# Optimization experiments

Measured on AMD Instinct MI355X. Metric: run time of the kernel, lower is better.

The kernel has to match this reference:

```python
import jax, jax.numpy as jnp
import numpy as np

N, K, D = 65536, 1024, 256
COMMIT = 0.25
EPS = 1e-12


def setup_inputs() -> dict:
    key = jax.random.key(0)
    kx, kw = jax.random.split(key)
    x = jax.random.normal(kx, (N, D), dtype=jnp.float32)
    # nn.Embedding weight init: uniform(-1/vector_num, 1/vector_num)
    weight = jax.random.uniform(kw, (K, D), dtype=jnp.float32,
                                minval=-1.0 / K, maxval=1.0 / K)
    return {"x": x, "weight": weight}


def reference(x, weight):
    distances = (jnp.sum(x * x, axis=1, keepdims=True)
                 + jnp.sum(weight * weight, axis=1)
                 - 2.0 * (x @ weight.T))
    vector_indices = jnp.argmin(distances, axis=1)              # [N]
    quantized = weight[vector_indices]                          # gather == one-hot @ weight

    e_latent_loss = jnp.mean((jax.lax.stop_gradient(quantized) - x) ** 2)
    q_latent_loss = jnp.mean((quantized - jax.lax.stop_gradient(x)) ** 2)
    quant_loss = q_latent_loss + COMMIT * e_latent_loss

    # straight-through estimator
    quantized_out = x + jax.lax.stop_gradient(quantized - x)

    # utilization: counts of each code (== column sums of one-hot encodings)
    counts = jnp.zeros((K,), x.dtype).at[vector_indices].add(1.0)
    util_loss = jnp.mean(jnp.abs(counts - x.shape[0] / K))

    # compactness: 2 * mean of pairwise euclidean distances among codebook rows
    sq = jnp.sum(weight * weight, axis=1)
    pd2 = sq[:, None] + sq[None, :] - 2.0 * (weight @ weight.T)  # [K, K]
    iu = jnp.triu(jnp.ones((K, K), bool), 1)
    pd = jnp.sqrt(jnp.maximum(jnp.where(iu, pd2, 1.0), EPS))
    n_pairs = K * (K - 1) // 2
    compact_loss = 2.0 * jnp.sum(jnp.where(iu, pd, 0.0)) / n_pairs

    return quantized_out, quant_loss, util_loss, compact_loss, vector_indices
```

## Files before the change

kernel.cpp:

```cpp
#include <hip/hip_runtime.h>
#include <math.h>

#define NROWS 65536
#define KCODES 1024
#define DDIM 256
#define ND_TOT (NROWS * DDIM)

#define WS_IDX      0
#define WS_COUNTS   262144
#define WS_SW       266240
#define WS_PARTQ    532480
#define WS_PARTP    536576
#define WS_FLAGCNT  540672
#define WS_FLAGLIST 540928
#define WS_WH       803072
#define WS_WL       1327360

typedef float f32x4 __attribute__((ext_vector_type(4)));
typedef short bf16x8 __attribute__((ext_vector_type(8)));

__device__ inline unsigned short f2bf(float f) {
  unsigned u = __float_as_uint(f);
  u += 0x7FFFu + ((u >> 16) & 1u);
  return (unsigned short)(u >> 16);
}
__device__ inline float bf2f(unsigned short h) {
  return __uint_as_float(((unsigned)h) << 16);
}

__device__ inline void gload16(const void* g, void* l) {
  __builtin_amdgcn_global_load_lds((const __attribute__((address_space(1))) void*)g,
                                   (__attribute__((address_space(3))) void*)l, 16, 0, 0);
}

__global__ __launch_bounds__(256) void vq_prep(const float* __restrict__ x,
                                               const float* __restrict__ w,
                                               unsigned short* __restrict__ xh,
                                               unsigned short* __restrict__ xl,
                                               float* __restrict__ sw,
                                               unsigned short* __restrict__ wh,
                                               unsigned short* __restrict__ wl,
                                               int* __restrict__ counts,
                                               int* __restrict__ flagCnt) {
#pragma clang fp contract(off)
  const int b = blockIdx.x;
  const int t = threadIdx.x;
  if (b >= 2048) {
    const int lane = t & 63, wv = t >> 6;
    const int row = (b - 2048) * 4 + wv;
    const float* src = w + (size_t)row * DDIM;
    float4 v4 = *(const float4*)&src[lane * 4];
    float fv[4] = {v4.x, v4.y, v4.z, v4.w};
    union { unsigned short us[4]; uint2 v; } ph, pl;
#pragma unroll
    for (int e = 0; e < 4; ++e) {
      unsigned short h = f2bf(fv[e]);
      ph.us[e] = h;
      pl.us[e] = f2bf(fv[e] - bf2f(h));
    }
    *(uint2*)&wh[(size_t)row * DDIM + lane * 4] = ph.v;
    *(uint2*)&wl[(size_t)row * DDIM + lane * 4] = pl.v;
    float acc = 0.f;
    if (lane < 16) {
      const float* p = src + ((lane >> 3) & 1) * 128 + (lane & 7);
      float v = p[0];
      acc = v * v;
      for (int k = 1; k < 16; ++k) { float vv = p[k * 8]; float e = vv * vv; acc = acc + e; }
    }
    acc = acc + __shfl_xor(acc, 1);
    acc = acc + __shfl_xor(acc, 2);
    acc = acc + __shfl_xor(acc, 4);
    const float hb = __shfl(acc, 8);
    if (lane == 0) sw[row] = acc + hb;
    return;
  }
  if (b == 0) {
#pragma unroll
    for (int j = 0; j < 4; ++j) counts[j * 256 + t] = 0;
    if (t == 0) flagCnt[0] = 0;
  }
  const size_t tid = (size_t)b * 256 + t;
  float4 a[4], c[4];
#pragma unroll
  for (int g = 0; g < 4; ++g) {
    const size_t e = ((size_t)g * 524288 + tid) * 8;
    a[g] = *(const float4*)&x[e];
    c[g] = *(const float4*)&x[e + 4];
  }
#pragma unroll
  for (int g = 0; g < 4; ++g) {
    const size_t e = ((size_t)g * 524288 + tid) * 8;
    float fv[8] = {a[g].x, a[g].y, a[g].z, a[g].w, c[g].x, c[g].y, c[g].z, c[g].w};
    union { unsigned short us[8]; uint4 v; } ph, pl;
#pragma unroll
    for (int k = 0; k < 8; ++k) {
      unsigned short h = f2bf(fv[k]);
      ph.us[k] = h;
      pl.us[k] = f2bf(fv[k] - bf2f(h));
    }
    *(uint4*)&xh[e] = ph.v;
    *(uint4*)&xl[e] = pl.v;
  }
}

#define TRM 128
#define BKM 64
#define REPAIR_T 1.5e-4f

__global__ __launch_bounds__(256, 2) void vq_argmin_mfma(
    const unsigned short* __restrict__ xh, const unsigned short* __restrict__ xl,
    const unsigned short* __restrict__ wh, const unsigned short* __restrict__ wl,
    const float* __restrict__ sw,
    int* __restrict__ idxOut, float* __restrict__ idxOutF,
    int* __restrict__ flagCnt, int* __restrict__ flagList) {
  __shared__ __align__(16) unsigned short lds_wh[TRM * BKM];
  __shared__ __align__(16) unsigned short lds_wl[TRM * BKM];
  __shared__ __align__(16) float sws[KCODES];
  __shared__ float mrgB1[TRM];
  __shared__ float mrgB2[TRM];
  __shared__ int   mrgI[TRM];

  const int t = threadIdx.x;
  const int lane = t & 63, wv = t >> 6;
  const int row0 = blockIdx.x * TRM;

  { f32x4 v = ((const f32x4*)sw)[t]; ((f32x4*)sws)[t] = v; }

  const int laneRow = lane >> 3;
  const int srcswz = ((lane & 7) * 16) ^ ((laneRow & 7) << 4);
  const char* whB = (const char*)wh;
  const char* wlB = (const char*)wl;

  bf16x8 ah[2][8], al[2][8];
  {
    const int rbase = row0 + wv * 32 + (lane & 15);
    const int kof = ((lane >> 4) & 3) * 8;
#pragma unroll
    for (int i = 0; i < 2; ++i)
#pragma unroll
      for (int ks = 0; ks < 8; ++ks) {
        const size_t e = (size_t)(rbase + i * 16) * DDIM + (size_t)(ks * 32 + kof);
        ah[i][ks] = *(const bf16x8*)&xh[e];
        al[i][ks] = *(const bf16x8*)&xl[e];
      }
  }

  float b1[8], b2[8];
  int bi[8];
#pragma unroll
  for (int s = 0; s < 8; ++s) { b1[s] = 3.4e38f; b2[s] = 3.4e38f; bi[s] = 0; }

  for (int ct = 0; ct < KCODES / TRM; ++ct) {
    f32x4 acc[2][8];
#pragma unroll
    for (int i = 0; i < 2; ++i)
#pragma unroll
      for (int j = 0; j < 8; ++j) acc[i][j] = (f32x4){0.f, 0.f, 0.f, 0.f};

    for (int dt = 0; dt < 4; ++dt) {
      __syncthreads();
#pragma unroll
      for (int i = 0; i < 4; ++i) {
        const int rb = wv * 32 + i * 8;
        const size_t gow = (size_t)(ct * 128 + rb + laneRow) * 512 + (size_t)(dt * 128 + srcswz);
        gload16(whB + gow, (char*)lds_wh + rb * 128);
        gload16(wlB + gow, (char*)lds_wl + rb * 128);
      }
      __syncthreads();

#pragma unroll
      for (int kh = 0; kh < 2; ++kh) {
        const int kb = kh * 64 + ((lane >> 4) & 3) * 16;
        const int ks = dt * 2 + kh;
#pragma unroll
        for (int j = 0; j < 8; ++j) {
          const int c = j * 16 + (lane & 15);
          const int off = c * 128 + (kb ^ ((c & 7) << 4));
          bf16x8 bh = *(const bf16x8*)((const char*)lds_wh + off);
          bf16x8 bl = *(const bf16x8*)((const char*)lds_wl + off);
#pragma unroll
          for (int i = 0; i < 2; ++i) {
            acc[i][j] = __builtin_amdgcn_mfma_f32_16x16x32_bf16(ah[i][ks], bh, acc[i][j], 0, 0, 0);
            acc[i][j] = __builtin_amdgcn_mfma_f32_16x16x32_bf16(ah[i][ks], bl, acc[i][j], 0, 0, 0);
            acc[i][j] = __builtin_amdgcn_mfma_f32_16x16x32_bf16(al[i][ks], bh, acc[i][j], 0, 0, 0);
          }
        }
      }
    }

#pragma unroll
    for (int j = 0; j < 8; ++j) {
      const int colbase = ct * 128 + j * 16 + (lane & 15);
      const float swv = sws[colbase];
#pragma unroll
      for (int i = 0; i < 2; ++i)
#pragma unroll
        for (int q = 0; q < 4; ++q) {
          const int s = i * 4 + q;
          const float e = fmaf(-2.f, acc[i][j][q], swv);
          const bool c1 = e < b1[s];
          b2[s] = c1 ? b1[s] : fminf(b2[s], e);
          bi[s] = c1 ? colbase : bi[s];
          b1[s] = fminf(b1[s], e);
        }
    }
  }

#pragma unroll
  for (int off = 1; off < 16; off <<= 1) {
#pragma unroll
    for (int s = 0; s < 8; ++s) {
      const float ob1 = __shfl_xor(b1[s], off);
      const float ob2 = __shfl_xor(b2[s], off);
      const int oi = __shfl_xor(bi[s], off);
      const float hi = fmaxf(b1[s], ob1);
      const bool take = ob1 < b1[s];
      b1[s] = fminf(b1[s], ob1);
      b2[s] = fminf(hi, fminf(b2[s], ob2));
      bi[s] = take ? oi : bi[s];
    }
  }
  if ((lane & 15) == 0) {
#pragma unroll
    for (int i = 0; i < 2; ++i)
#pragma unroll
      for (int q = 0; q < 4; ++q) {
        const int s = i * 4 + q;
        const int r = wv * 32 + i * 16 + ((lane >> 4) & 3) * 4 + q;
        mrgB1[r] = b1[s]; mrgB2[r] = b2[s]; mrgI[r] = bi[s];
      }
  }
  __syncthreads();
  if (t < TRM) {
    const float b1f = mrgB1[t];
    const float b2f = mrgB2[t];
    const int idxf = mrgI[t];
    const int grow = row0 + t;
    idxOut[grow] = idxf;
    idxOutF[grow] = (float)idxf;
    const bool flag = (b2f - b1f) < REPAIR_T;
    unsigned long long m = __ballot(flag);
    int base2 = 0;
    if ((t & 63) == 0) base2 = atomicAdd(flagCnt, __popcll(m));
    base2 = __shfl(base2, 0);
    if (flag) flagList[base2 + __popcll(m & ((1ull << (t & 63)) - 1ull))] = grow;
  }
}

#define RPB 8
__global__ __launch_bounds__(256) void vq_repair_compact(
    const float* __restrict__ x, const float* __restrict__ w,
    const float* __restrict__ sw,
    const int* __restrict__ flagCnt, const int* __restrict__ flagList,
    int* __restrict__ idxOut, float* __restrict__ idxOutF,
    float* __restrict__ partialP) {
  const int t = threadIdx.x;
  const int lane = t & 63, wvid = t >> 6;
  if (blockIdx.x >= 1024) {
    const int i = blockIdx.x - 1024;
    __shared__ float wi[DDIM];
    wi[t] = w[(size_t)i * DDIM + t];
    __syncthreads();
    float swi = sw[i];
    double s = 0.0;
    for (int j = i + 1 + t; j < KCODES; j += 256) {
      const float4* wj = (const float4*)(w + (size_t)j * DDIM);
      const float4* wi4 = (const float4*)wi;
      float acc = 0.f;
#pragma unroll 8
      for (int d4 = 0; d4 < DDIM / 4; ++d4) {
        float4 a = wi4[d4];
        float4 b = wj[d4];
        acc += a.x * b.x + a.y * b.y + a.z * b.z + a.w * b.w;
      }
      float pd2 = (swi + sw[j]) - 2.0f * acc;
      s += (double)sqrtf(fmaxf(pd2, 1e-12f));
    }
    for (int off = 32; off > 0; off >>= 1) s += __shfl_down(s, off);
    __shared__ double redc[4];
    if (lane == 0) redc[wvid] = s;
    __syncthreads();
    if (t == 0)
      partialP[i] = (float)(redc[0] + redc[1] + redc[2] + redc[3]);
    return;
  }
  __shared__ __align__(16) float xrow[RPB][DDIM];
  __shared__ float sxsh[RPB];
  __shared__ float redD[RPB][4];
  __shared__ int   redI[RPB][4];
  const int cnt = flagCnt[0];
  for (int base = blockIdx.x * RPB; base < cnt; base += 1024 * RPB) {
    const int nr = min(RPB, cnt - base);
    __syncthreads();
    for (int r = 0; r < nr; ++r)
      xrow[r][t] = x[(size_t)flagList[base + r] * DDIM + t];
    __syncthreads();
    if (t < nr) {
#pragma clang fp contract(off)
      float halves[2];
#pragma unroll
      for (int h = 0; h < 2; ++h) {
        const float* p = &xrow[t][h * 128];
        float acc[8];
#pragma unroll
        for (int j = 0; j < 8; ++j) { float v = p[j]; acc[j] = v * v; }
        for (int i = 8; i < 128; i += 8) {
#pragma unroll
          for (int j = 0; j < 8; ++j) { float v = p[i + j]; float e = v * v; acc[j] = acc[j] + e; }
        }
        halves[h] = ((acc[0] + acc[1]) + (acc[2] + acc[3])) + ((acc[4] + acc[5]) + (acc[6] + acc[7]));
      }
      sxsh[t] = halves[0] + halves[1];
    }
    __syncthreads();
    float acc[4][RPB];
#pragma unroll
    for (int g = 0; g < 4; ++g)
#pragma unroll
      for (int r = 0; r < RPB; ++r) acc[g][r] = 0.f;
    const float4* wrp0 = (const float4*)(w + (size_t)(0 * 256 + t) * DDIM);
    const float4* wrp1 = (const float4*)(w + (size_t)(1 * 256 + t) * DDIM);
    const float4* wrp2 = (const float4*)(w + (size_t)(2 * 256 + t) * DDIM);
    const float4* wrp3 = (const float4*)(w + (size_t)(3 * 256 + t) * DDIM);
    for (int d4 = 0; d4 < DDIM / 4; ++d4) {
      float4 xr4[RPB];
#pragma unroll
      for (int r = 0; r < RPB; ++r) xr4[r] = *(const float4*)&xrow[r][d4 * 4];
      const float4 wv0 = wrp0[d4], wv1 = wrp1[d4], wv2 = wrp2[d4], wv3 = wrp3[d4];
#pragma unroll
      for (int e = 0; e < 4; ++e) {
        const float w0 = (e == 0) ? wv0.x : (e == 1) ? wv0.y : (e == 2) ? wv0.z : wv0.w;
        const float w1 = (e == 0) ? wv1.x : (e == 1) ? wv1.y : (e == 2) ? wv1.z : wv1.w;
        const float w2 = (e == 0) ? wv2.x : (e == 1) ? wv2.y : (e == 2) ? wv2.z : wv2.w;
        const float w3 = (e == 0) ? wv3.x : (e == 1) ? wv3.y : (e == 2) ? wv3.z : wv3.w;
#pragma unroll
        for (int r = 0; r < RPB; ++r) {
          const float xv = (e == 0) ? xr4[r].x : (e == 1) ? xr4[r].y : (e == 2) ? xr4[r].z : xr4[r].w;
          acc[0][r] = fmaf(xv, w0, acc[0][r]);
          acc[1][r] = fmaf(xv, w1, acc[1][r]);
          acc[2][r] = fmaf(xv, w2, acc[2][r]);
          acc[3][r] = fmaf(xv, w3, acc[3][r]);
        }
      }
    }
    float bD[RPB]; int bI[RPB];
#pragma unroll
    for (int r = 0; r < RPB; ++r) { bD[r] = 3.4e38f; bI[r] = 0x7fffffff; }
#pragma unroll
    for (int g = 0; g < 4; ++g) {
      const int c = g * 256 + t;
      const float swc = sw[c];
#pragma unroll
      for (int r = 0; r < RPB; ++r) {
        const float tt = sxsh[r] + swc;
        const float dist = tt - 2.0f * acc[g][r];
        if (dist < bD[r]) { bD[r] = dist; bI[r] = c; }
      }
    }
#pragma unroll
    for (int off = 32; off > 0; off >>= 1) {
#pragma unroll
      for (int r = 0; r < RPB; ++r) {
        const float od = __shfl_down(bD[r], off);
        const int oi = __shfl_down(bI[r], off);
        if (od < bD[r] || (od == bD[r] && oi < bI[r])) { bD[r] = od; bI[r] = oi; }
      }
    }
    if (lane == 0) {
#pragma unroll
      for (int r = 0; r < RPB; ++r) { redD[r][wvid] = bD[r]; redI[r][wvid] = bI[r]; }
    }
    __syncthreads();
    if (t < nr) {
      float bb = redD[t][0]; int bix = redI[t][0];
#pragma unroll
      for (int k = 1; k < 4; ++k) {
        const float od = redD[t][k]; const int oi = redI[t][k];
        if (od < bb || (od == bb && oi < bix)) { bb = od; bix = oi; }
      }
      const int row = flagList[base + t];
      idxOut[row] = bix;
      idxOutF[row] = (float)bix;
    }
  }
}

__global__ __launch_bounds__(256) void vq_quantize(const float* __restrict__ x,
                                                   const float* __restrict__ w,
                                                   const int* __restrict__ idxArr,
                                                   float* __restrict__ qout,
                                                   int* __restrict__ counts,
                                                   float* __restrict__ partialQ) {
  const int wave = threadIdx.x >> 6;
  const int lane = threadIdx.x & 63;
  const int base = blockIdx.x * 64 + wave * 16;
  float s = 0.f;
#pragma unroll
  for (int rg = 0; rg < 4; ++rg) {
    int idx4[4];
#pragma unroll
    for (int r = 0; r < 4; ++r) idx4[r] = idxArr[base + rg * 4 + r];
    float4 xv[4], qv[4];
#pragma unroll
    for (int r = 0; r < 4; ++r) {
      xv[r] = ((const float4*)(x + (size_t)(base + rg * 4 + r) * DDIM))[lane];
      qv[r] = ((const float4*)(w + (size_t)idx4[r] * DDIM))[lane];
    }
#pragma unroll
    for (int r = 0; r < 4; ++r) {
      const int row = base + rg * 4 + r;
      float dx = qv[r].x - xv[r].x, dy = qv[r].y - xv[r].y;
      float dz = qv[r].z - xv[r].z, dw = qv[r].w - xv[r].w;
      float4 o;
      o.x = xv[r].x + dx; o.y = xv[r].y + dy; o.z = xv[r].z + dz; o.w = xv[r].w + dw;
      ((float4*)(qout + (size_t)row * DDIM))[lane] = o;
      s += dx * dx + dy * dy + dz * dz + dw * dw;
      if (lane == 0) atomicAdd(&counts[idx4[r]], 1);
    }
  }
  double d = s;
  for (int off = 32; off > 0; off >>= 1) d += __shfl_down(d, off);
  __shared__ double red[4];
  if (lane == 0) red[wave] = d;
  __syncthreads();
  if (threadIdx.x == 0)
    partialQ[blockIdx.x] = (float)(red[0] + red[1] + red[2] + red[3]);
}

__global__ __launch_bounds__(1024) void vq_final(const float* __restrict__ partialQ,
                                                 const float* __restrict__ partialP,
                                                 const int* __restrict__ counts,
                                                 float* __restrict__ out) {
  const int t = threadIdx.x;
  const int lane = t & 63, wave = t >> 6;
  double q = (double)partialQ[t];
  double p = (double)partialP[t];
  double u = (double)fabsf((float)counts[t] - 64.0f);
  for (int off = 32; off > 0; off >>= 1) {
    q += __shfl_down(q, off);
    p += __shfl_down(p, off);
    u += __shfl_down(u, off);
  }
  __shared__ double redQ[16], redP[16], redU[16];
  if (lane == 0) { redQ[wave] = q; redP[wave] = p; redU[wave] = u; }
  __syncthreads();
  if (t == 0) {
    double sq = 0, sp = 0, su = 0;
    for (int j = 0; j < 16; ++j) { sq += redQ[j]; sp += redP[j]; su += redU[j]; }
    float m = (float)(sq / 16777216.0);
    out[ND_TOT] = m + 0.25f * m;
    out[ND_TOT + 1] = (float)(su / 1024.0);
    out[ND_TOT + 2] = (float)(2.0 * sp / 523776.0);
  }
}

extern "C" void kernel_launch(void* const* d_in, const int* in_sizes, int n_in,
                              void* d_out, int out_size, void* d_ws, size_t ws_size,
                              hipStream_t stream) {
  const float* x = (const float*)d_in[0];
  const float* w = (const float*)d_in[1];
  float* out = (float*)d_out;

  char* ws = (char*)d_ws;
  int* wsIdx    = (int*)(ws + WS_IDX);
  int* counts   = (int*)(ws + WS_COUNTS);
  float* swv    = (float*)(ws + WS_SW);
  float* partQ  = (float*)(ws + WS_PARTQ);
  float* partP  = (float*)(ws + WS_PARTP);
  int* flagCnt  = (int*)(ws + WS_FLAGCNT);
  int* flagList = (int*)(ws + WS_FLAGLIST);
  unsigned short* whS = (unsigned short*)(ws + WS_WH);
  unsigned short* wlS = (unsigned short*)(ws + WS_WL);

  unsigned short* xhS = (unsigned short*)d_out;
  unsigned short* xlS = xhS + (size_t)ND_TOT;

  vq_prep<<<2304, 256, 0, stream>>>(x, w, xhS, xlS, swv, whS, wlS, counts, flagCnt);
  vq_argmin_mfma<<<NROWS / TRM, 256, 0, stream>>>(xhS, xlS, whS, wlS, swv,
                                                  wsIdx, out + ND_TOT + 3, flagCnt, flagList);
  vq_repair_compact<<<2048, 256, 0, stream>>>(x, w, swv, flagCnt, flagList,
                                              wsIdx, out + ND_TOT + 3, partP);
  vq_quantize<<<1024, 256, 0, stream>>>(x, w, wsIdx, out, counts, partQ);
  vq_final<<<1, 1024, 0, stream>>>(partQ, partP, counts, out);
}
```

Before: 256.0 us.

## Split codebook compactness into tiled 32x32 upper-triangle kernel separate from repair

Moves the pairwise codebook-distance computation out of the combined repair kernel into its own kernel. The new kernel covers the upper-triangular 32x32 tile pairs (528 blocks), stages both tiles in LDS and gives each thread a 2x2 register micro-tile, replacing the old one-row-per-block loop that re-read codebook rows from global memory with unbalanced work. It zeroes all 1024 partialP slots in prep so the final reduction sees zeros beyond block 528. The cost is one extra kernel launch, and the repair kernel now runs alone at 1024 blocks.

```diff
diff --git a/kernel.cpp b/kernel.cpp
--- a/kernel.cpp
+++ b/kernel.cpp
@@ -41,7 +41,8 @@
                                                unsigned short* __restrict__ wh,
                                                unsigned short* __restrict__ wl,
                                                int* __restrict__ counts,
-                                               int* __restrict__ flagCnt) {
+                                               int* __restrict__ flagCnt,
+                                               float* __restrict__ partialP) {
 #pragma clang fp contract(off)
   const int b = blockIdx.x;
   const int t = threadIdx.x;
@@ -76,7 +77,7 @@
   }
   if (b == 0) {
 #pragma unroll
-    for (int j = 0; j < 4; ++j) counts[j * 256 + t] = 0;
+    for (int j = 0; j < 4; ++j) { counts[j * 256 + t] = 0; partialP[j * 256 + t] = 0.f; }
     if (t == 0) flagCnt[0] = 0;
   }
   const size_t tid = (size_t)b * 256 + t;
@@ -248,42 +249,13 @@
 }
 
 #define RPB 8
-__global__ __launch_bounds__(256) void vq_repair_compact(
+__global__ __launch_bounds__(256) void vq_repair(
     const float* __restrict__ x, const float* __restrict__ w,
     const float* __restrict__ sw,
     const int* __restrict__ flagCnt, const int* __restrict__ flagList,
-    int* __restrict__ idxOut, float* __restrict__ idxOutF,
-    float* __restrict__ partialP) {
+    int* __restrict__ idxOut, float* __restrict__ idxOutF) {
   const int t = threadIdx.x;
   const int lane = t & 63, wvid = t >> 6;
-  if (blockIdx.x >= 1024) {
-    const int i = blockIdx.x - 1024;
-    __shared__ float wi[DDIM];
-    wi[t] = w[(size_t)i * DDIM + t];
-    __syncthreads();
-    float swi = sw[i];
-    double s = 0.0;
-    for (int j = i + 1 + t; j < KCODES; j += 256) {
-      const float4* wj = (const float4*)(w + (size_t)j * DDIM);
-      const float4* wi4 = (const float4*)wi;
-      float acc = 0.f;
-#pragma unroll 8
-      for (int d4 = 0; d4 < DDIM / 4; ++d4) {
-        float4 a = wi4[d4];
-        float4 b = wj[d4];
-        acc += a.x * b.x + a.y * b.y + a.z * b.z + a.w * b.w;
-      }
-      float pd2 = (swi + sw[j]) - 2.0f * acc;
-      s += (double)sqrtf(fmaxf(pd2, 1e-12f));
-    }
-    for (int off = 32; off > 0; off >>= 1) s += __shfl_down(s, off);
-    __shared__ double redc[4];
-    if (lane == 0) redc[wvid] = s;
-    __syncthreads();
-    if (t == 0)
-      partialP[i] = (float)(redc[0] + redc[1] + redc[2] + redc[3]);
-    return;
-  }
   __shared__ __align__(16) float xrow[RPB][DDIM];
   __shared__ float sxsh[RPB];
   __shared__ float redD[RPB][4];
@@ -385,6 +357,63 @@
   }
 }
 
+#define CTI 32
+#define CPAD 260
+__global__ __launch_bounds__(256) void vq_compact(const float* __restrict__ w,
+                                                  const float* __restrict__ sw,
+                                                  float* __restrict__ partialP) {
+  __shared__ __align__(16) float wI[CTI][CPAD];
+  __shared__ __align__(16) float wJ[CTI][CPAD];
+  const int t = threadIdx.x;
+  const int lane = t & 63, wvid = t >> 6;
+  int b = blockIdx.x, ti = 0;
+  while (b >= 32 - ti) { b -= 32 - ti; ++ti; }
+  const int tj = ti + b;
+#pragma unroll
+  for (int k = 0; k < 8; ++k) {
+    const int q = k * 256 + t;
+    const int r = q >> 6, c4 = q & 63;
+    float4 vI = *(const float4*)&w[(size_t)(ti * CTI + r) * DDIM + c4 * 4];
+    float4 vJ = *(const float4*)&w[(size_t)(tj * CTI + r) * DDIM + c4 * 4];
+    *(float4*)&wI[r][c4 * 4] = vI;
+    *(float4*)&wJ[r][c4 * 4] = vJ;
+  }
+  __syncthreads();
+  const int ia = 2 * (t & 15);
+  const int jc = 2 * (t >> 4);
+  float a00 = 0.f, a01 = 0.f, a10 = 0.f, a11 = 0.f;
+  for (int d4 = 0; d4 < DDIM / 4; ++d4) {
+    const float4 A0 = *(const float4*)&wI[ia][d4 * 4];
+    const float4 A1 = *(const float4*)&wI[ia + 1][d4 * 4];
+    const float4 B0 = *(const float4*)&wJ[jc][d4 * 4];
+    const float4 B1 = *(const float4*)&wJ[jc + 1][d4 * 4];
+    a00 += A0.x * B0.x + A0.y * B0.y + A0.z * B0.z + A0.w * B0.w;
+    a01 += A0.x * B1.x + A0.y * B1.y + A0.z * B1.z + A0.w * B1.w;
+    a10 += A1.x * B0.x + A1.y * B0.y + A1.z * B0.z + A1.w * B0.w;
+    a11 += A1.x * B1.x + A1.y * B1.y + A1.z * B1.z + A1.w * B1.w;
+  }
+  double s = 0.0;
+  {
+    const int i0 = ti * CTI + ia, j0 = tj * CTI + jc;
+    const float acc2[2][2] = {{a00, a01}, {a10, a11}};
+#pragma unroll
+    for (int ii = 0; ii < 2; ++ii)
+#pragma unroll
+      for (int jj = 0; jj < 2; ++jj) {
+        const int i = i0 + ii, j = j0 + jj;
+        if (i < j) {
+          const float pd2 = (sw[i] + sw[j]) - 2.0f * acc2[ii][jj];
+          s += (double)sqrtf(fmaxf(pd2, 1e-12f));
+        }
+      }
+  }
+  for (int off = 32; off > 0; off >>= 1) s += __shfl_down(s, off);
+  __shared__ double redc[4];
+  if (lane == 0) redc[wvid] = s;
+  __syncthreads();
+  if (t == 0) partialP[blockIdx.x] = (float)(redc[0] + redc[1] + redc[2] + redc[3]);
+}
+
 __global__ __launch_bounds__(256) void vq_quantize(const float* __restrict__ x,
                                                    const float* __restrict__ w,
                                                    const int* __restrict__ idxArr,
@@ -475,11 +504,11 @@
   unsigned short* xhS = (unsigned short*)d_out;
   unsigned short* xlS = xhS + (size_t)ND_TOT;
 
-  vq_prep<<<2304, 256, 0, stream>>>(x, w, xhS, xlS, swv, whS, wlS, counts, flagCnt);
+  vq_prep<<<2304, 256, 0, stream>>>(x, w, xhS, xlS, swv, whS, wlS, counts, flagCnt, partP);
   vq_argmin_mfma<<<NROWS / TRM, 256, 0, stream>>>(xhS, xlS, whS, wlS, swv,
                                                   wsIdx, out + ND_TOT + 3, flagCnt, flagList);
-  vq_repair_compact<<<2048, 256, 0, stream>>>(x, w, swv, flagCnt, flagList,
-                                              wsIdx, out + ND_TOT + 3, partP);
+  vq_repair<<<1024, 256, 0, stream>>>(x, w, swv, flagCnt, flagList, wsIdx, out + ND_TOT + 3);
+  vq_compact<<<528, 256, 0, stream>>>(w, swv, partP);
   vq_quantize<<<1024, 256, 0, stream>>>(x, w, wsIdx, out, counts, partQ);
   vq_final<<<1, 1024, 0, stream>>>(partQ, partP, counts, out);
 }
```

Result: faster. 236.6 us (-7.6%).

## Tile codebook pairwise-distance computation and move it into prep kernel

Applied to the files above, without the earlier changes.

Moves the compactness pairwise-distance computation out of the repair kernel and into the prep kernel as 2080 extra blocks. Each block handles a 16x16 tile of codebook pairs staged in shared memory, so the 1024x1024 triangle is no longer computed row-by-row with uncoalesced global reads. Partial sums are accumulated with float atomics into a buffer that is zeroed beforehand by a memset. The squared norms are recomputed per pair, so the extra FLOPs are traded for independence from the sw buffer.

```diff
diff --git a/kernel.cpp b/kernel.cpp
--- a/kernel.cpp
+++ b/kernel.cpp
@@ -41,10 +41,51 @@
                                                unsigned short* __restrict__ wh,
                                                unsigned short* __restrict__ wl,
                                                int* __restrict__ counts,
-                                               int* __restrict__ flagCnt) {
+                                               int* __restrict__ flagCnt,
+                                               float* __restrict__ partialP) {
 #pragma clang fp contract(off)
   const int b = blockIdx.x;
   const int t = threadIdx.x;
+  if (b >= 2304) {
+    __shared__ __align__(16) float wI[16][260];
+    __shared__ __align__(16) float wJ[16][260];
+    int tb = b - 2304, ti = 0;
+    while (tb >= 64 - ti) { tb -= 64 - ti; ++ti; }
+    const int tj = ti + tb;
+    const int lane = t & 63, wvid = t >> 6;
+#pragma unroll
+    for (int k = 0; k < 4; ++k) {
+      const int q = k * 256 + t;
+      const int r = q >> 6, c4 = q & 63;
+      float4 vI = *(const float4*)&w[(size_t)(ti * 16 + r) * DDIM + c4 * 4];
+      float4 vJ = *(const float4*)&w[(size_t)(tj * 16 + r) * DDIM + c4 * 4];
+      *(float4*)&wI[r][c4 * 4] = vI;
+      *(float4*)&wJ[r][c4 * 4] = vJ;
+    }
+    __syncthreads();
+    const int ii = t & 15, jj = t >> 4;
+    const int gi = ti * 16 + ii, gj = tj * 16 + jj;
+    double s = 0.0;
+    if (gi < gj) {
+      float dot = 0.f, sqa = 0.f, sqb = 0.f;
+      for (int d4 = 0; d4 < DDIM / 4; ++d4) {
+        const float4 A = *(const float4*)&wI[ii][d4 * 4];
+        const float4 B = *(const float4*)&wJ[jj][d4 * 4];
+        dot += A.x * B.x + A.y * B.y + A.z * B.z + A.w * B.w;
+        sqa += A.x * A.x + A.y * A.y + A.z * A.z + A.w * A.w;
+        sqb += B.x * B.x + B.y * B.y + B.z * B.z + B.w * B.w;
+      }
+      const float pd2 = (sqa + sqb) - 2.0f * dot;
+      s = (double)sqrtf(fmaxf(pd2, 1e-12f));
+    }
+    for (int off = 32; off > 0; off >>= 1) s += __shfl_down(s, off);
+    __shared__ double redc[4];
+    if (lane == 0) redc[wvid] = s;
+    __syncthreads();
+    if (t == 0)
+      atomicAdd(&partialP[(b - 2304) & 1023], (float)(redc[0] + redc[1] + redc[2] + redc[3]));
+    return;
+  }
   if (b >= 2048) {
     const int lane = t & 63, wv = t >> 6;
     const int row = (b - 2048) * 4 + wv;
@@ -248,42 +289,13 @@
 }
 
 #define RPB 8
-__global__ __launch_bounds__(256) void vq_repair_compact(
+__global__ __launch_bounds__(256) void vq_repair(
     const float* __restrict__ x, const float* __restrict__ w,
     const float* __restrict__ sw,
     const int* __restrict__ flagCnt, const int* __restrict__ flagList,
-    int* __restrict__ idxOut, float* __restrict__ idxOutF,
-    float* __restrict__ partialP) {
+    int* __restrict__ idxOut, float* __restrict__ idxOutF) {
   const int t = threadIdx.x;
   const int lane = t & 63, wvid = t >> 6;
-  if (blockIdx.x >= 1024) {
-    const int i = blockIdx.x - 1024;
-    __shared__ float wi[DDIM];
-    wi[t] = w[(size_t)i * DDIM + t];
-    __syncthreads();
-    float swi = sw[i];
-    double s = 0.0;
-    for (int j = i + 1 + t; j < KCODES; j += 256) {
-      const float4* wj = (const float4*)(w + (size_t)j * DDIM);
-      const float4* wi4 = (const float4*)wi;
-      float acc = 0.f;
-#pragma unroll 8
-      for (int d4 = 0; d4 < DDIM / 4; ++d4) {
-        float4 a = wi4[d4];
-        float4 b = wj[d4];
-        acc += a.x * b.x + a.y * b.y + a.z * b.z + a.w * b.w;
-      }
-      float pd2 = (swi + sw[j]) - 2.0f * acc;
-      s += (double)sqrtf(fmaxf(pd2, 1e-12f));
-    }
-    for (int off = 32; off > 0; off >>= 1) s += __shfl_down(s, off);
-    __shared__ double redc[4];
-    if (lane == 0) redc[wvid] = s;
-    __syncthreads();
-    if (t == 0)
-      partialP[i] = (float)(redc[0] + redc[1] + redc[2] + redc[3]);
-    return;
-  }
   __shared__ __align__(16) float xrow[RPB][DDIM];
   __shared__ float sxsh[RPB];
   __shared__ float redD[RPB][4];
@@ -475,11 +487,12 @@
   unsigned short* xhS = (unsigned short*)d_out;
   unsigned short* xlS = xhS + (size_t)ND_TOT;
 
-  vq_prep<<<2304, 256, 0, stream>>>(x, w, xhS, xlS, swv, whS, wlS, counts, flagCnt);
+  hipMemsetAsync(ws + WS_PARTP, 0, 4096, stream);
+
+  vq_prep<<<4384, 256, 0, stream>>>(x, w, xhS, xlS, swv, whS, wlS, counts, flagCnt, partP);
   vq_argmin_mfma<<<NROWS / TRM, 256, 0, stream>>>(xhS, xlS, whS, wlS, swv,
                                                   wsIdx, out + ND_TOT + 3, flagCnt, flagList);
-  vq_repair_compact<<<2048, 256, 0, stream>>>(x, w, swv, flagCnt, flagList,
-                                              wsIdx, out + ND_TOT + 3, partP);
+  vq_repair<<<1024, 256, 0, stream>>>(x, w, swv, flagCnt, flagList, wsIdx, out + ND_TOT + 3);
   vq_quantize<<<1024, 256, 0, stream>>>(x, w, wsIdx, out, counts, partQ);
   vq_final<<<1, 1024, 0, stream>>>(partQ, partP, counts, out);
 }
```

Result: faster. 249.9 us (-2.4%).
